# Kernel tuning notes

Measured on AMD Instinct MI355X. Metric: run time of the kernel, lower is better.

Reference implementation:

```python
import jax, jax.numpy as jnp
import numpy as np

B, L, E = 4, 1024, 1024
H = 16
HD = E // H
CLIP = 16
SCALE = 1.0 / np.sqrt(HD)


def setup_inputs() -> dict:
    key = jax.random.key(0)
    ks = jax.random.split(key, 13)
    def lin(k, fan_in, fan_out, gain):
        # xavier_uniform
        limit = gain * np.sqrt(6.0 / (fan_in + fan_out))
        return jax.random.uniform(k, (fan_out, fan_in), jnp.float32, -limit, limit)
    inv_sqrt2 = 1.0 / np.sqrt(2.0)
    return {
        "query": jax.random.normal(ks[0], (B, L, E), jnp.float32),
        "key": jax.random.normal(ks[1], (B, L, E), jnp.float32),
        "value": jax.random.normal(ks[2], (B, L, E), jnp.float32),
        "wq": lin(ks[3], E, E, inv_sqrt2), "bq": jnp.zeros((E,), jnp.float32),
        "wk": lin(ks[4], E, E, inv_sqrt2), "bk": jnp.zeros((E,), jnp.float32),
        "wv": lin(ks[5], E, E, inv_sqrt2), "bv": jnp.zeros((E,), jnp.float32),
        "wo": lin(ks[6], E, E, 1.0), "bo": jnp.zeros((E,), jnp.float32),
        "rel_k": jax.random.normal(ks[7], (2 * CLIP + 1, HD), jnp.float32) * 0.02,
        "rel_v": jax.random.normal(ks[8], (2 * CLIP + 1, HD), jnp.float32) * 0.02,
    }


def _heads(x):  # (B, L, E) -> (B, H, L, HD)
    return x.reshape(B, L, H, HD).transpose(0, 2, 1, 3)


def reference(query, key, value, wq, bq, wk, bk, wv, bv, wo, bo, rel_k, rel_v):
    q = _heads(query @ wq.T + bq)
    k = _heads(key @ wk.T + bk)
    v = _heads(value @ wv.T + bv)

    # relative-position index matrix (L_q, L_k), clipped to [-CLIP, CLIP]
    pos = jnp.arange(L)
    dist = jnp.clip(pos[None, :] - pos[:, None], -CLIP, CLIP) + CLIP
    r_k = rel_k[dist]  # (L, L, HD)
    r_v = rel_v[dist]  # (L, L, HD)

    dot = jnp.einsum('bhid,bhjd->bhij', q, k)
    rel = jnp.einsum('bhid,ijd->bhij', q, r_k)
    scores = (dot + rel) * SCALE
    attn = jax.nn.softmax(scores, axis=-1)

    y = jnp.einsum('bhij,bhjd->bhid', attn, v) + jnp.einsum('bhij,ijd->bhid', attn, r_v)
    y = y.transpose(0, 2, 1, 3).reshape(B, L, E)
    return y @ wo.T + bo
```

## Files before the change

kernel.cpp:

```cpp
#include <hip/hip_runtime.h>

#define BB 4
#define LL 1024
#define EE 1024
#define HH 16
#define HD 64
#define NBUCKET 33
#define SCALE 0.125f
#define SC2 (0.125f * 1.44269504088896f)

typedef unsigned short u16;
using f32x4 = __attribute__((ext_vector_type(4))) float;
using s16x8 = __attribute__((ext_vector_type(8))) short;

__device__ __forceinline__ u16 f2bf(float f) {
  union { float f; unsigned u; } x; x.f = f;
  unsigned r = (x.u + 0x7fffu + ((x.u >> 16) & 1u)) >> 16;
  return (u16)r;
}

__device__ __forceinline__ void gld_lds16(const void* g, void* s) {
  __builtin_amdgcn_global_load_lds((const __attribute__((address_space(1))) void*)g,
                                   (__attribute__((address_space(3))) void*)s, 16, 0, 0);
}

__global__ __launch_bounds__(256) void cvt_all(
    const float* __restrict__ q, const float* __restrict__ k, const float* __restrict__ v,
    const float* __restrict__ wq, const float* __restrict__ wk, const float* __restrict__ wv,
    const float* __restrict__ wo, const float* __restrict__ rk,
    u16* __restrict__ oq, u16* __restrict__ ok, u16* __restrict__ ov,
    u16* __restrict__ owq, u16* __restrict__ owk, u16* __restrict__ owv,
    u16* __restrict__ owo, u16* __restrict__ ork) {
  const int bid = blockIdx.x;
  const int tid = threadIdx.x;
  if (bid < 12288) {
    const int z = bid >> 12;
    const int i = (bid & 4095) * 256 + tid;
    const float* in = z == 0 ? q : (z == 1 ? k : v);
    u16* out = z == 0 ? oq : (z == 1 ? ok : ov);
    float4 f = ((const float4*)in)[i];
    ushort4 o;
    o.x = f2bf(f.x); o.y = f2bf(f.y); o.z = f2bf(f.z); o.w = f2bf(f.w);
    ((ushort4*)out)[i] = o;
  } else if (bid < 16384) {
    const int z = (bid - 12288) >> 10;
    const int i = ((bid - 12288) & 1023) * 256 + tid;
    const float* in = z == 0 ? wq : (z == 1 ? wk : (z == 2 ? wv : wo));
    u16* out = z == 0 ? owq : (z == 1 ? owk : (z == 2 ? owv : owo));
    float4 f = ((const float4*)in)[i];
    ushort4 o;
    o.x = f2bf(f.x); o.y = f2bf(f.y); o.z = f2bf(f.z); o.w = f2bf(f.w);
    ((ushort4*)out)[i] = o;
  } else {
    const int i = (bid - 16384) * 256 + tid;
    ork[i] = (i < 33 * 64) ? f2bf(rk[i]) : (u16)0;
  }
}

template <int MODE>
__device__ __forceinline__ void gemm128_dbuf(u16* __restrict__ sm,
                                             const u16* __restrict__ A,
                                             const u16* __restrict__ Bw,
                                             const float* __restrict__ bias,
                                             u16* __restrict__ obf,
                                             float* __restrict__ ofp,
                                             int N, int K, int m0, int n0) {
  const int tid = threadIdx.x;
  const int wave = tid >> 6, lane = tid & 63;
  const int row16 = lane & 15, quad = lane >> 4;
  const int wr = (wave >> 1) * 64, wc = (wave & 1) * 64;
  const int srow = lane >> 3, scol = (lane & 7) * 8;
  const int rsw = (row16 & 7) * 8;

  f32x4 acc[4][4] = {};

  auto stage = [&](int k0, u16* as, u16* bs) {
#pragma unroll
    for (int t = 0; t < 4; ++t) {
      const int chunk = wave * 4 + t;
      const int r = chunk * 8 + srow;
      const int cs = scol ^ ((r & 7) * 8);
      gld_lds16(A + (size_t)(m0 + r) * K + k0 + cs, as + chunk * 512);
      gld_lds16(Bw + (size_t)(n0 + r) * K + k0 + cs, bs + chunk * 512);
    }
  };

  stage(0, sm, sm + 8192);
  asm volatile("s_waitcnt vmcnt(0)" ::: "memory");
  __builtin_amdgcn_s_barrier();
  __builtin_amdgcn_sched_barrier(0);

  const int NK = K >> 6;
  for (int kt = 0; kt < NK; ++kt) {
    u16* as = sm + (kt & 1) * 16384;
    u16* bs = as + 8192;
    if (kt + 1 < NK) {
      u16* an = sm + ((kt + 1) & 1) * 16384;
      stage((kt + 1) << 6, an, an + 8192);
    }
#pragma unroll
    for (int ks = 0; ks < 2; ++ks) {
      const int cfs = (ks * 32 + quad * 8) ^ rsw;
      s16x8 af[4], bf[4];
#pragma unroll
      for (int mi = 0; mi < 4; ++mi)
        af[mi] = *(const s16x8*)&as[(wr + mi * 16 + row16) * 64 + cfs];
#pragma unroll
      for (int ni = 0; ni < 4; ++ni)
        bf[ni] = *(const s16x8*)&bs[(wc + ni * 16 + row16) * 64 + cfs];
#pragma unroll
      for (int mi = 0; mi < 4; ++mi)
#pragma unroll
        for (int ni = 0; ni < 4; ++ni)
          acc[mi][ni] = __builtin_amdgcn_mfma_f32_16x16x32_bf16(af[mi], bf[ni], acc[mi][ni], 0, 0, 0);
    }
    asm volatile("s_waitcnt vmcnt(0) lgkmcnt(0)" ::: "memory");
    __builtin_amdgcn_s_barrier();
    __builtin_amdgcn_sched_barrier(0);
  }

#pragma unroll
  for (int mi = 0; mi < 4; ++mi)
#pragma unroll
    for (int ni = 0; ni < 4; ++ni) {
      const int n = n0 + wc + ni * 16 + row16;
      const float bn = bias[n];
      if (MODE == 2) {
        const int mr0 = m0 + wr + mi * 16 + quad * 4;
        const int b = mr0 >> 10, l = mr0 & 1023;
        const int h = n >> 6, hd = n & 63;
        ushort4 o;
        o.x = f2bf(acc[mi][ni][0] + bn);
        o.y = f2bf(acc[mi][ni][1] + bn);
        o.z = f2bf(acc[mi][ni][2] + bn);
        o.w = f2bf(acc[mi][ni][3] + bn);
        *(ushort4*)&obf[((size_t)((b * HH + h) * HD + hd)) * LL + l] = o;
      } else if (MODE == 0) {
#pragma unroll
        for (int r = 0; r < 4; ++r) {
          const int m = m0 + wr + mi * 16 + quad * 4 + r;
          const float v = acc[mi][ni][r] + bn;
          const int b = m >> 10, l = m & 1023, h = n >> 6, hd = n & 63;
          obf[((size_t)((b * HH + h) * LL + l)) * HD + hd] = f2bf(v);
        }
      } else {
#pragma unroll
        for (int r = 0; r < 4; ++r) {
          const int m = m0 + wr + mi * 16 + quad * 4 + r;
          ofp[(size_t)m * N + n] = acc[mi][ni][r] + bn;
        }
      }
    }
}

__global__ __launch_bounds__(256) void proj_gemm(
    const u16* __restrict__ xq, const u16* __restrict__ xk, const u16* __restrict__ xv,
    const u16* __restrict__ wqb, const u16* __restrict__ wkb, const u16* __restrict__ wvb,
    const float* __restrict__ bq, const float* __restrict__ bk, const float* __restrict__ bv,
    u16* __restrict__ oq, u16* __restrict__ ok, u16* __restrict__ ovt) {
  __shared__ u16 sm[4 * 8192];
  const int work = (blockIdx.x & 7) * 96 + (blockIdx.x >> 3);
  const int z = work >> 8;
  const int m0 = ((work & 255) >> 3) * 128;
  const int n0 = (work & 7) * 128;
  if (z == 0)
    gemm128_dbuf<0>(sm, xq, wqb, bq, oq, nullptr, EE, EE, m0, n0);
  else if (z == 1)
    gemm128_dbuf<0>(sm, xk, wkb, bk, ok, nullptr, EE, EE, m0, n0);
  else
    gemm128_dbuf<2>(sm, xv, wvb, bv, ovt, nullptr, EE, EE, m0, n0);
}

__global__ __launch_bounds__(256) void out_gemm(const u16* __restrict__ Y,
                                                const u16* __restrict__ wob,
                                                const float* __restrict__ bo,
                                                float* __restrict__ out) {
  __shared__ u16 sm[4 * 8192];
  const int work = (blockIdx.x & 7) * 32 + (blockIdx.x >> 3);
  const int m0 = (work >> 3) * 128;
  const int n0 = (work & 7) * 128;
  gemm128_dbuf<1>(sm, Y, wob, bo, nullptr, out, EE, EE, m0, n0);
}

__global__ __launch_bounds__(256) void attn_fused(
    const u16* __restrict__ Q, const u16* __restrict__ Kb, const u16* __restrict__ Vt,
    const u16* __restrict__ RKp, const float* __restrict__ RV, u16* __restrict__ Y) {
  __shared__ __align__(16) float qr_sm[4][576];
  __shared__ __align__(16) float s_sm[4][16 * 36];
  __shared__ __align__(16) unsigned char kv[16384];

  const int tid = threadIdx.x;
  const int wave = tid >> 6, lane = tid & 63;
  const int row16 = lane & 15, quad = lane >> 4;
  const int bh = blockIdx.x & 63;
  const int i0 = (blockIdx.x >> 6) * 64;
  const int wq0 = i0 + wave * 16;
  const u16* qp = Q + (size_t)bh * LL * HD;
  const char* kpB = (const char*)(Kb + (size_t)bh * LL * HD);
  const char* vpB = (const char*)(Vt + (size_t)bh * HD * LL);

  float* qr_w = &qr_sm[wave][0];
  float* s_w = &s_sm[wave][0];

  int srcK[2], srcV[2];
#pragma unroll
  for (int t = 0; t < 2; ++t) {
    const int cK = (wave * 2 + t) * 64 + lane;
    const int rw = cK >> 3;
    const int cb = ((cK * 16) & 127) ^ ((rw & 7) << 4);
    srcK[t] = rw * 128 + cb;
    srcV[t] = rw * 2048 + cb;
  }
  const int q2 = row16 >> 2;
  const int prow = ((((q2 << 1) | (q2 >> 1)) & 3) << 2) + (row16 & 3);
  const int swzK = (prow & 7) << 4;
  const int swzV = (row16 & 7) << 4;
  const int rho4 = (((quad << 1) | (quad >> 1)) & 3) << 2;

#pragma unroll
  for (int t = 0; t < 2; ++t) {
    gld_lds16(kpB + srcK[t], kv + (wave * 2 + t) * 1024);
    gld_lds16(vpB + srcV[t], kv + 8192 + (wave * 2 + t) * 1024);
  }

  for (int t = lane; t < 16 * 36; t += 64) s_w[t] = 0.f;

  s16x8 qf[2];
#pragma unroll
  for (int ks = 0; ks < 2; ++ks)
    qf[ks] = *(const s16x8*)(qp + (size_t)(wq0 + row16) * HD + ks * 32 + quad * 8);

  f32x4 a0, a2;
#pragma unroll
  for (int nt = 0; nt < 3; ++nt) {
    f32x4 a = {};
#pragma unroll
    for (int ks = 0; ks < 2; ++ks) {
      s16x8 afr = *(const s16x8*)(RKp + (size_t)(nt * 16 + row16) * HD + ks * 32 + quad * 8);
      a = __builtin_amdgcn_mfma_f32_16x16x32_bf16(afr, qf[ks], a, 0, 0, 0);
    }
    if (nt == 0) a0 = a;
    if (nt == 2) a2 = a;
#pragma unroll
    for (int r = 0; r < 4; ++r) {
      const int bk = nt * 16 + quad * 4 + r;
      if (bk < NBUCKET) qr_w[bk * 17 + row16] = a[r];
    }
  }
  const float blo = __shfl(a0[0], row16);
  const float bhi = __shfl(a2[0], row16);

  f32x4 oacc[4] = {};
  float rsum = 0.f, plos = 0.f, phis = 0.f;
  int baseg[4];
#pragma unroll
  for (int g = 0; g < 4; ++g) baseg[g] = g * 16 + rho4 - wq0 - row16;

  asm volatile("s_waitcnt vmcnt(0) lgkmcnt(0)" ::: "memory");
  __builtin_amdgcn_s_barrier();
  __builtin_amdgcn_sched_barrier(0);

  for (int jt = 0; jt < 16; ++jt) {
    const int j0 = jt * 64;

    s16x8 kreg[2], vreg[2];
    if (jt < 15) {
      const size_t j1 = (size_t)(j0 + 64);
#pragma unroll
      for (int t = 0; t < 2; ++t) {
        kreg[t] = *(const s16x8*)(kpB + j1 * 128 + srcK[t]);
        vreg[t] = *(const s16x8*)(vpB + j1 * 2 + srcV[t]);
      }
    }

    f32x4 sacc[4] = {};
    __builtin_amdgcn_s_setprio(1);
#pragma unroll
    for (int ks = 0; ks < 2; ++ks)
#pragma unroll
      for (int g = 0; g < 4; ++g) {
        const int L = (g * 16 + prow) * 128 + ks * 64 + quad * 16;
        const s16x8 kfr = *(const s16x8*)(kv + (L ^ swzK));
        sacc[g] = __builtin_amdgcn_mfma_f32_16x16x32_bf16(kfr, qf[ks], sacc[g], 0, 0, 0);
      }
    __builtin_amdgcn_s_setprio(0);

    unsigned pk[4][2];
    const bool far_lo = (wq0 >= j0 + 79);
    const bool far_hi = (j0 >= wq0 + 31);
    if (far_lo || far_hi) {
      const float bb = (far_lo ? blo : bhi) * SC2;
      float tacc = 0.f;
#pragma unroll
      for (int g = 0; g < 4; ++g)
#pragma unroll
        for (int rr = 0; rr < 2; ++rr) {
          const float pv0 = __builtin_amdgcn_exp2f(sacc[g][rr * 2] * SC2 + bb);
          const float pv1 = __builtin_amdgcn_exp2f(sacc[g][rr * 2 + 1] * SC2 + bb);
          tacc += pv0 + pv1;
          unsigned c;
          asm("v_cvt_pk_bf16_f32 %0, %1, %2" : "=v"(c) : "v"(pv0), "v"(pv1));
          pk[g][rr] = c;
        }
      rsum += tacc;
      if (far_lo) plos += tacc; else phis += tacc;
    } else {
#pragma unroll
      for (int g = 0; g < 4; ++g)
#pragma unroll
        for (int rr = 0; rr < 2; ++rr) {
          float pv2[2];
#pragma unroll
          for (int e = 0; e < 2; ++e) {
            const int r = rr * 2 + e;
            const int dr = baseg[g] + j0 + r;
            int bk = dr < -16 ? -16 : (dr > 16 ? 16 : dr);
            bk += 16;
            const float bias = qr_w[bk * 17 + row16];
            const float pv = __builtin_amdgcn_exp2f((sacc[g][r] + bias) * SC2);
            pv2[e] = pv;
            rsum += pv;
            if (dr <= -16) plos += pv;
            else if (dr >= 16) phis += pv;
            else atomicAdd(&s_w[row16 * 36 + bk], pv);
          }
          unsigned c;
          asm("v_cvt_pk_bf16_f32 %0, %1, %2" : "=v"(c) : "v"(pv2[0]), "v"(pv2[1]));
          pk[g][rr] = c;
        }
    }

    s16x8 pf[2];
#pragma unroll
    for (int ks = 0; ks < 2; ++ks) {
      unsigned x0 = pk[ks * 2][0], y0 = pk[ks * 2 + 1][0];
      unsigned x1 = pk[ks * 2][1], y1 = pk[ks * 2 + 1][1];
      asm("v_permlane32_swap_b32 %0, %1" : "+v"(x0), "+v"(y0));
      asm("v_permlane32_swap_b32 %0, %1" : "+v"(x1), "+v"(y1));
      union { unsigned u[4]; s16x8 v; } pfu;
      pfu.u[0] = x0; pfu.u[1] = x1; pfu.u[2] = y0; pfu.u[3] = y1;
      pf[ks] = pfu.v;
    }

    __builtin_amdgcn_s_setprio(1);
#pragma unroll
    for (int ks = 0; ks < 2; ++ks)
#pragma unroll
      for (int dt = 0; dt < 4; ++dt) {
        const int L = (dt * 16 + row16) * 128 + ks * 64 + quad * 16;
        const s16x8 vfr = *(const s16x8*)(kv + 8192 + (L ^ swzV));
        oacc[dt] = __builtin_amdgcn_mfma_f32_16x16x32_bf16(vfr, pf[ks], oacc[dt], 0, 0, 0);
      }
    __builtin_amdgcn_s_setprio(0);

    asm volatile("s_waitcnt lgkmcnt(0)" ::: "memory");
    __builtin_amdgcn_s_barrier();
    __builtin_amdgcn_sched_barrier(0);

    if (jt < 15) {
#pragma unroll
      for (int t = 0; t < 2; ++t) {
        *(s16x8*)(kv + (wave * 2 + t) * 1024 + lane * 16) = kreg[t];
        *(s16x8*)(kv + 8192 + (wave * 2 + t) * 1024 + lane * 16) = vreg[t];
      }
      asm volatile("s_waitcnt lgkmcnt(0)" ::: "memory");
      __builtin_amdgcn_s_barrier();
      __builtin_amdgcn_sched_barrier(0);
    }
  }

  float t1 = rsum + __shfl_xor(rsum, 16);
  const float lacc = t1 + __shfl_xor(t1, 32);
  t1 = plos + __shfl_xor(plos, 16);
  const float slo = t1 + __shfl_xor(t1, 32);
  t1 = phis + __shfl_xor(phis, 16);
  const float shi = t1 + __shfl_xor(t1, 32);

  float* rv_sm = (float*)kv;
  for (int t = tid; t < NBUCKET * HD; t += 256) rv_sm[t] = RV[t];
  __syncthreads();

  const int b = bh >> 4, h = bh & 15;
  float rel[4][4] = {};
  for (int bk = 0; bk < NBUCKET; ++bk) {
    float sv = s_w[row16 * 36 + bk];
    if (bk == 0) sv += slo;
    if (bk == 32) sv += shi;
#pragma unroll
    for (int dt = 0; dt < 4; ++dt) {
      const f32x4 rv4 = *(const f32x4*)&rv_sm[bk * HD + dt * 16 + quad * 4];
#pragma unroll
      for (int r = 0; r < 4; ++r) rel[dt][r] += sv * rv4[r];
    }
  }
  const float inv = 1.0f / lacc;
#pragma unroll
  for (int dt = 0; dt < 4; ++dt) {
    ushort4 o;
    o.x = f2bf((oacc[dt][0] + rel[dt][0]) * inv);
    o.y = f2bf((oacc[dt][1] + rel[dt][1]) * inv);
    o.z = f2bf((oacc[dt][2] + rel[dt][2]) * inv);
    o.w = f2bf((oacc[dt][3] + rel[dt][3]) * inv);
    *(ushort4*)&Y[((size_t)(b * LL + wq0 + row16)) * EE + h * HD + dt * 16 + quad * 4] = o;
  }
}

extern "C" void kernel_launch(void* const* d_in, const int* in_sizes, int n_in,
                              void* d_out, int out_size, void* d_ws, size_t ws_size,
                              hipStream_t stream) {
  const float* query = (const float*)d_in[0];
  const float* key_  = (const float*)d_in[1];
  const float* value = (const float*)d_in[2];
  const float* wq = (const float*)d_in[3];
  const float* bq = (const float*)d_in[4];
  const float* wk = (const float*)d_in[5];
  const float* bk = (const float*)d_in[6];
  const float* wv = (const float*)d_in[7];
  const float* bv = (const float*)d_in[8];
  const float* wo = (const float*)d_in[9];
  const float* bo = (const float*)d_in[10];
  const float* rel_k = (const float*)d_in[11];
  const float* rel_v = (const float*)d_in[12];

  char* base = (char*)d_ws;
  size_t off = 0;
  auto alloc = [&](size_t bytes) -> void* {
    void* p = base + off;
    off += (bytes + 255) & ~(size_t)255;
    return p;
  };
  const size_t XE = (size_t)BB * LL * EE;
  u16* xq    = (u16*)alloc(XE * 2);
  u16* xk    = (u16*)alloc(XE * 2);
  u16* xv    = (u16*)alloc(XE * 2);
  u16* wqb   = (u16*)alloc((size_t)EE * EE * 2);
  u16* wkb   = (u16*)alloc((size_t)EE * EE * 2);
  u16* wvb   = (u16*)alloc((size_t)EE * EE * 2);
  u16* wob   = (u16*)alloc((size_t)EE * EE * 2);
  u16* q_ws  = (u16*)alloc(XE * 2);
  u16* k_ws  = (u16*)alloc(XE * 2);
  u16* vt_ws = (u16*)alloc(XE * 2);
  u16* relkp = (u16*)alloc(48 * 64 * 2);
  u16* y_ws = xq;

  cvt_all<<<16396, 256, 0, stream>>>(query, key_, value, wq, wk, wv, wo, rel_k,
                                     xq, xk, xv, wqb, wkb, wvb, wob, relkp);

  proj_gemm<<<768, 256, 0, stream>>>(
      xq, xk, xv, wqb, wkb, wvb, bq, bk, bv, q_ws, k_ws, vt_ws);

  attn_fused<<<1024, 256, 0, stream>>>(q_ws, k_ws, vt_ws, relkp, rel_v, y_ws);

  out_gemm<<<256, 256, 0, stream>>>(y_ws, wob, bo, (float*)d_out);
}
```

Measured before the change: 230.6 us.

## Use dedicated 64x128-tile output GEMM kernel to double block count

Replaces the shared 128x128 GEMM template for the output projection with a specialized kernel using 64x128 tiles and 512 blocks instead of 256. The goal is better occupancy across the CUs on a small 4096x1024x1024 GEMM, where 256 blocks underfill the device. Removes the fp32-output mode from the template. Smaller tiles reduce data reuse per block and raise the total number of global loads.

```diff
diff --git a/kernel.cpp b/kernel.cpp
--- a/kernel.cpp
+++ b/kernel.cpp
@@ -135,19 +135,13 @@
         o.z = f2bf(acc[mi][ni][2] + bn);
         o.w = f2bf(acc[mi][ni][3] + bn);
         *(ushort4*)&obf[((size_t)((b * HH + h) * HD + hd)) * LL + l] = o;
-      } else if (MODE == 0) {
+      } else {
 #pragma unroll
         for (int r = 0; r < 4; ++r) {
           const int m = m0 + wr + mi * 16 + quad * 4 + r;
           const float v = acc[mi][ni][r] + bn;
           const int b = m >> 10, l = m & 1023, h = n >> 6, hd = n & 63;
           obf[((size_t)((b * HH + h) * LL + l)) * HD + hd] = f2bf(v);
-        }
-      } else {
-#pragma unroll
-        for (int r = 0; r < 4; ++r) {
-          const int m = m0 + wr + mi * 16 + quad * 4 + r;
-          ofp[(size_t)m * N + n] = acc[mi][ni][r] + bn;
         }
       }
     }
@@ -171,15 +165,87 @@
     gemm128_dbuf<2>(sm, xv, wvb, bv, ovt, nullptr, EE, EE, m0, n0);
 }
 
-__global__ __launch_bounds__(256) void out_gemm(const u16* __restrict__ Y,
-                                                const u16* __restrict__ wob,
+__global__ __launch_bounds__(256) void out_gemm(const u16* __restrict__ A,
+                                                const u16* __restrict__ Bw,
                                                 const float* __restrict__ bo,
                                                 float* __restrict__ out) {
-  __shared__ u16 sm[4 * 8192];
-  const int work = (blockIdx.x & 7) * 32 + (blockIdx.x >> 3);
-  const int m0 = (work >> 3) * 128;
+  __shared__ u16 sm[2 * 12288];
+  const int work = (blockIdx.x & 7) * 64 + (blockIdx.x >> 3);
+  const int m0 = (work >> 3) * 64;
   const int n0 = (work & 7) * 128;
-  gemm128_dbuf<1>(sm, Y, wob, bo, nullptr, out, EE, EE, m0, n0);
+  const int K = EE, N = EE;
+
+  const int tid = threadIdx.x;
+  const int wave = tid >> 6, lane = tid & 63;
+  const int row16 = lane & 15, quad = lane >> 4;
+  const int wm = (wave >> 1) * 32, wn = (wave & 1) * 64;
+  const int srow = lane >> 3, scol = (lane & 7) * 8;
+  const int rsw = (row16 & 7) * 8;
+
+  f32x4 acc[2][4] = {};
+
+  auto stage = [&](int k0, u16* as, u16* bs) {
+#pragma unroll
+    for (int t = 0; t < 2; ++t) {
+      const int chunk = wave * 2 + t;
+      const int r = chunk * 8 + srow;
+      const int cs = scol ^ ((r & 7) * 8);
+      gld_lds16(A + (size_t)(m0 + r) * K + k0 + cs, as + chunk * 512);
+    }
+#pragma unroll
+    for (int t = 0; t < 4; ++t) {
+      const int chunk = wave * 4 + t;
+      const int r = chunk * 8 + srow;
+      const int cs = scol ^ ((r & 7) * 8);
+      gld_lds16(Bw + (size_t)(n0 + r) * K + k0 + cs, bs + chunk * 512);
+    }
+  };
+
+  stage(0, sm, sm + 4096);
+  asm volatile("s_waitcnt vmcnt(0)" ::: "memory");
+  __builtin_amdgcn_s_barrier();
+  __builtin_amdgcn_sched_barrier(0);
+
+  for (int kt = 0; kt < 16; ++kt) {
+    u16* as = sm + (kt & 1) * 12288;
+    u16* bs = as + 4096;
+    if (kt + 1 < 16) {
+      u16* an = sm + ((kt + 1) & 1) * 12288;
+      stage((kt + 1) << 6, an, an + 4096);
+    }
+#pragma unroll
+    for (int ks = 0; ks < 2; ++ks) {
+      const int cfs = (ks * 32 + quad * 8) ^ rsw;
+      s16x8 af[2], bf[4];
+#pragma unroll
+      for (int mi = 0; mi < 2; ++mi)
+        af[mi] = *(const s16x8*)&as[(wm + mi * 16 + row16) * 64 + cfs];
+#pragma unroll
+      for (int ni = 0; ni < 4; ++ni)
+        bf[ni] = *(const s16x8*)&bs[(wn + ni * 16 + row16) * 64 + cfs];
+#pragma unroll
+      for (int mi = 0; mi < 2; ++mi)
+#pragma unroll
+        for (int ni = 0; ni < 4; ++ni)
+          acc[mi][ni] = __builtin_amdgcn_mfma_f32_16x16x32_bf16(af[mi], bf[ni], acc[mi][ni], 0, 0, 0);
+    }
+    asm volatile("s_waitcnt vmcnt(0) lgkmcnt(0)" ::: "memory");
+    __builtin_amdgcn_s_barrier();
+    __builtin_amdgcn_sched_barrier(0);
+  }
+
+#pragma unroll
+  for (int mi = 0; mi < 2; ++mi)
+#pragma unroll
+    for (int ni = 0; ni < 4; ++ni) {
+      const int n = n0 + wn + ni * 16 + row16;
+      const float bn = bo[n];
+#pragma unroll
+      for (int r = 0; r < 4; ++r) {
+        const int m = m0 + wm + mi * 16 + quad * 4 + r;
+        out[(size_t)m * N + n] = acc[mi][ni][r] + bn;
+      }
+    }
 }
 
 __global__ __launch_bounds__(256) void attn_fused(
@@ -451,5 +517,5 @@
 
   attn_fused<<<1024, 256, 0, stream>>>(q_ws, k_ws, vt_ws, relkp, rel_v, y_ws);
 
-  out_gemm<<<256, 256, 0, stream>>>(y_ws, wob, bo, (float*)d_out);
-}
+  out_gemm<<<512, 256, 0, stream>>>(y_ws, wob, bo, (float*)d_out);
+}
```

After: 225.9 us (median of 2 runs). -2.0%, faster.
